# Optimization experiments

Hardware: AMD Instinct MI355X
Metric: run time of the kernel (lower is better)

## Reference

```python
import jax, jax.numpy as jnp
import numpy as np

ATTN_HEADS = 4
NEG = -1e9
LN_EPS = 1e-5


def _ln(x, s, b):
    m = x.mean(-1, keepdims=True)
    v = ((x - m) ** 2).mean(-1, keepdims=True)
    return (x - m) * jax.lax.rsqrt(v + LN_EPS) * s + b


def setup_inputs() -> dict:
    key = jax.random.key(0)
    ks = jax.random.split(key, 40)
    B, L, D, FF, NL = 512, 192, 256, 1024, 2
    V, U, I = 30000, 100000, 50000
    Lp, Ln, NF = 30, 300, 13
    Lu = jax.random.randint(ks[0], (B,), 1, L // 2)
    Li = jax.random.randint(ks[1], (B,), 1, L // 2)
    inp = {
        'attr': jax.random.randint(ks[2], (B, L), 0, V),
        'attr_inds': jax.random.randint(ks[3], (B, L), 0, 3),
        'attr_tf': jax.random.uniform(ks[4], (B, L), dtype=jnp.float32),
        'attr_feat': jax.random.normal(ks[5], (B, L, NF), dtype=jnp.float32),
        'attr_lens': Lu + Li,
        'attr_lens_user': Lu,
        'attr_lens_item': Li,
        'user_ids': jax.random.randint(ks[6], (B,), 0, U),
        'item_ids': jax.random.randint(ks[7], (B,), 0, I),
        'pos_targets': jax.random.randint(ks[8], (B, Lp), 0, V),
        'pos_lens': jax.random.randint(ks[9], (B,), 1, Lp + 1),
        'neg_targets': jax.random.randint(ks[10], (B, Ln), 0, V),
        'neg_lens': jax.random.randint(ks[11], (B,), 1, Ln + 1),
        # embedding tables (uniform(-0.1,0.1) per f_init_weight)
        'attr_emb': jax.random.uniform(ks[12], (V, D), minval=-0.1, maxval=0.1),
        'ind_emb': jax.random.uniform(ks[13], (3, D), minval=-0.1, maxval=0.1),
        'user_emb_table': jax.random.uniform(ks[14], (U, D), minval=-0.1, maxval=0.1),
        'item_emb_table': jax.random.uniform(ks[15], (I, D), minval=-0.1, maxval=0.1),
        'out_emb_user': jax.random.uniform(ks[16], (V, 2 * D), minval=-0.1, maxval=0.1),
        'out_emb_item': jax.random.uniform(ks[17], (V, 2 * D), minval=-0.1, maxval=0.1),
        # attr-weight head: Linear(13,1) + sigmoid
        'feat_w': jax.random.normal(ks[18], (NF,)) * 0.02,
        'feat_b': jnp.zeros(()),
        # transformer encoder params, stacked over NL layers
        'Wqkv': jax.random.normal(ks[19], (NL, 3 * D, D)) * 0.02,
        'bqkv': jnp.zeros((NL, 3 * D)),
        'Wo': jax.random.normal(ks[20], (NL, D, D)) * 0.02,
        'bo': jnp.zeros((NL, D)),
        'ln1_s': jnp.ones((NL, D)), 'ln1_b': jnp.zeros((NL, D)),
        'W1': jax.random.normal(ks[21], (NL, FF, D)) * 0.02,
        'b1': jnp.zeros((NL, FF)),
        'W2': jax.random.normal(ks[22], (NL, D, FF)) * 0.02,
        'b2': jnp.zeros((NL, D)),
        'ln2_s': jnp.ones((NL, D)), 'ln2_b': jnp.zeros((NL, D)),
    }
    return inp


def reference(attr, attr_inds, attr_tf, attr_feat, attr_lens, attr_lens_user,
              attr_lens_item, user_ids, item_ids, pos_targets, pos_lens,
              neg_targets, neg_lens, attr_emb, ind_emb, user_emb_table,
              item_emb_table, out_emb_user, out_emb_item, feat_w, feat_b,
              Wqkv, bqkv, Wo, bo, ln1_s, ln1_b, W1, b1, W2, b2, ln2_s, ln2_b):
    B, L = attr.shape
    D = attr_emb.shape[1]
    NL = Wqkv.shape[0]
    Dh = D // ATTN_HEADS
    pos = jnp.arange(L)
    valid = pos[None, :] < attr_lens[:, None]  # [B,L] True = valid key

    x = attr_emb[attr] + ind_emb[attr_inds]  # [B,L,D]
    for l in range(NL):  # post-LN TransformerEncoderLayer, relu, no dropout
        qkv = x @ Wqkv[l].T + bqkv[l]
        q, k, v = jnp.split(qkv, 3, axis=-1)
        q = q.reshape(B, L, ATTN_HEADS, Dh).transpose(0, 2, 1, 3)
        k = k.reshape(B, L, ATTN_HEADS, Dh).transpose(0, 2, 1, 3)
        v = v.reshape(B, L, ATTN_HEADS, Dh).transpose(0, 2, 1, 3)
        scores = jnp.einsum('bhqd,bhkd->bhqk', q, k) / np.sqrt(Dh).astype(x.dtype)
        scores = jnp.where(valid[:, None, None, :], scores, NEG)
        a = jax.nn.softmax(scores, axis=-1)
        ctx = jnp.einsum('bhqk,bhkd->bhqd', a, v).transpose(0, 2, 1, 3).reshape(B, L, D)
        x = _ln(x + ctx @ Wo[l].T + bo[l], ln1_s[l], ln1_b[l])
        ff = jax.nn.relu(x @ W1[l].T + b1[l]) @ W2[l].T + b2[l]
        x = _ln(x + ff, ln2_s[l], ln2_b[l])

    # ragged weighted segment average over user span [0,Lu) and item span [Lu,Lu+Li)
    w_user = jax.nn.sigmoid(attr_feat @ feat_w + feat_b)  # [B,L]
    wted = x * attr_tf[..., None]
    umask = pos[None, :] < attr_lens_user[:, None]
    imask = (~umask) & (pos[None, :] < (attr_lens_user + attr_lens_item)[:, None])
    user_x = (wted * w_user[..., None] * umask[..., None]).sum(1) / attr_lens_user[:, None].astype(x.dtype)
    item_x = (wted * (1.0 - w_user)[..., None] * imask[..., None]).sum(1) / attr_lens_item[:, None].astype(x.dtype)

    user_out = jnp.concatenate([user_x, user_emb_table[user_ids]], axis=-1)  # [B,2D]
    item_out = jnp.concatenate([item_x, item_emb_table[item_ids]], axis=-1)

    def logit(t):
        return (jnp.einsum('bkd,bd->bk', out_emb_user[t], user_out)
                + jnp.einsum('bkd,bd->bk', out_emb_item[t], item_out))

    pos_logits = logit(pos_targets)
    neg_logits = logit(neg_targets)
    pmask = jnp.arange(pos_targets.shape[1])[None, :] < pos_lens[:, None]
    nmask = jnp.arange(neg_targets.shape[1])[None, :] < neg_lens[:, None]
    logits = jnp.concatenate([pos_logits, neg_logits], axis=-1)
    mask = jnp.concatenate([pmask, nmask], axis=-1)
    new_targets = jnp.concatenate([jnp.ones_like(pos_targets), jnp.zeros_like(neg_targets)], axis=1) * mask
    return logits, mask, new_targets
```

## Files before the change

kernel.cpp:

```cpp
#include <hip/hip_runtime.h>
#include <hip/hip_bf16.h>
#include <cstdint>
#include <cstddef>

#define B_ 512
#define L_ 192
#define D_ 256
#define H_ 4
#define DH_ 64
#define FF_ 1024
#define NL_ 2
#define LP_ 30
#define LNEG_ 300
#define NF_ 13
#define M_ (B_*L_)
#define NT_ 330
#define V_ 30000

typedef __attribute__((ext_vector_type(8))) short bf16x8;
typedef __attribute__((ext_vector_type(4))) float f32x4;

__device__ __forceinline__ ushort f2b(float f) {
  union { float f; uint32_t u; } v; v.f = f;
  uint32_t u = v.u;
  return (ushort)((u + 0x7FFFu + ((u >> 16) & 1u)) >> 16);
}
__device__ __forceinline__ float b2f(ushort u) {
  union { uint32_t u; float f; } v; v.u = (uint32_t)u << 16; return v.f;
}
__device__ __forceinline__ void stage16(const ushort* src, char* dst) {
  __builtin_amdgcn_global_load_lds((const __attribute__((address_space(1))) unsigned int*)src,
                                   (__attribute__((address_space(3))) unsigned int*)dst, 16, 0, 0);
}

__global__ __launch_bounds__(512) void k_prefix(
    const int* __restrict__ lens, int* __restrict__ off,
    int* __restrict__ ccnt, int* __restrict__ ccntp, int Bc, int nchunks)
{
  const int t = threadIdx.x;
  int s = 0;
  for (int i = 0; i < t; ++i) s += lens[i];
  off[t] = s;
  if (t == 511) off[512] = s + lens[511];
  if (t < nchunks) {
    int s2 = 0;
    const int c0 = t * Bc;
    for (int i = 0; i < Bc; ++i) s2 += lens[c0 + i];
    ccnt[t]  = s2;
    ccntp[t] = (s2 + 127) & ~127;
  }
}

__global__ __launch_bounds__(256) void k_f2b(const float* __restrict__ in, ushort* __restrict__ out) {
  const int i = (blockIdx.x*256 + threadIdx.x)*8;
  float4 a = *(const float4*)(in+i);
  float4 b = *(const float4*)(in+i+4);
  ushort4 o1; o1.x=f2b(a.x); o1.y=f2b(a.y); o1.z=f2b(a.z); o1.w=f2b(a.w);
  ushort4 o2; o2.x=f2b(b.x); o2.y=f2b(b.y); o2.z=f2b(b.z); o2.w=f2b(b.w);
  *(ushort4*)(out+i)   = o1;
  *(ushort4*)(out+i+4) = o2;
}

__global__ __launch_bounds__(256) void k_f2b4(
    const float* __restrict__ wq, const float* __restrict__ wo,
    const float* __restrict__ w1, const float* __restrict__ w2,
    ushort* __restrict__ oq, ushort* __restrict__ oo,
    ushort* __restrict__ o1, ushort* __restrict__ o2)
{
  int bb = blockIdx.x;
  const float* in; ushort* out; int base;
  if (bb < 192)      { in = wq; out = oq; base = bb; }
  else if (bb < 256) { in = wo; out = oo; base = bb - 192; }
  else if (bb < 512) { in = w1; out = o1; base = bb - 256; }
  else               { in = w2; out = o2; base = bb - 512; }
  const int i = base*2048 + threadIdx.x*8;
  float4 a = *(const float4*)(in+i);
  float4 b = *(const float4*)(in+i+4);
  ushort4 q1; q1.x=f2b(a.x); q1.y=f2b(a.y); q1.z=f2b(a.z); q1.w=f2b(a.w);
  ushort4 q2; q2.x=f2b(b.x); q2.y=f2b(b.y); q2.z=f2b(b.z); q2.w=f2b(b.w);
  *(ushort4*)(out+i)   = q1;
  *(ushort4*)(out+i+4) = q2;
}

__global__ __launch_bounds__(256) void k_embed(
    const int* __restrict__ attr, const int* __restrict__ inds,
    const int* __restrict__ lens, const int* __restrict__ off,
    const float* __restrict__ attr_emb, const float* __restrict__ ind_emb,
    ushort* __restrict__ xb)
{
  int idx = blockIdx.x*256 + threadIdx.x;
  int token = idx >> 6;
  int c = (idx & 63) * 4;
  int b = token / L_;
  int l = token - b*L_;
  if (l >= lens[b]) return;
  size_t crow = (size_t)off[b] + l;
  int a = attr[token];
  int id = inds[token];
  const float4 e  = *(const float4*)(attr_emb + (size_t)a*D_ + c);
  const float4 ie = *(const float4*)(ind_emb  + (size_t)id*D_ + c);
  ushort4 ob; ob.x=f2b(e.x+ie.x); ob.y=f2b(e.y+ie.y); ob.z=f2b(e.z+ie.z); ob.w=f2b(e.w+ie.w);
  *(ushort4*)(xb + crow*D_ + c) = ob;
}

template<int OUT_BF16, int RELU>
__global__ __launch_bounds__(256) void k_gemm_mfma(
    const ushort* __restrict__ A, const int* __restrict__ aoffp,
    const int* __restrict__ cntp,
    const ushort* __restrict__ W, const float* __restrict__ bias,
    void* __restrict__ Cv, int N, int K)
{
  if ((int)blockIdx.y * 128 >= *cntp) return;
  __shared__ alignas(16) ushort As[8192];
  __shared__ alignas(16) ushort Bs[8192];
  const int abase = *aoffp;
  const int tid = threadIdx.x;
  const int w = tid >> 6, l = tid & 63;
  const int g = l >> 4, c16 = l & 15;
  const int m0 = blockIdx.y*128, n0 = blockIdx.x*128;
  const int wr = w >> 1, wc = w & 1;
  const int swzr = (c16 & 7) << 4;

  f32x4 acc[4][4];
  #pragma unroll
  for (int i=0;i<4;++i)
    #pragma unroll
    for (int j=0;j<4;++j) acc[i][j] = (f32x4){0.f,0.f,0.f,0.f};

  for (int k0=0; k0<K; k0+=64) {
    #pragma unroll
    for (int i=0;i<4;++i) {
      const int li  = i*4096 + tid*16;
      const int row = li >> 7;
      const int col = ((li & 127) ^ ((row & 7) << 4)) >> 1;
      stage16(A + (size_t)(abase+m0+row)*K + k0 + col, (char*)(As) + i*4096 + w*1024);
      stage16(W + (size_t)(n0+row)*K + k0 + col,       (char*)(Bs) + i*4096 + w*1024);
    }
    __syncthreads();
    #pragma unroll
    for (int ks=0; ks<2; ++ks) {
      const int cb = ((g*16 + ks*64) ^ swzr) >> 1;
      bf16x8 af[4], bfr[4];
      #pragma unroll
      for (int i2=0;i2<4;++i2) {
        af[i2]  = *(const bf16x8*)(As + (size_t)(wr*64 + i2*16 + c16)*64 + cb);
        bfr[i2] = *(const bf16x8*)(Bs + (size_t)(wc*64 + i2*16 + c16)*64 + cb);
      }
      #pragma unroll
      for (int mi=0;mi<4;++mi)
        #pragma unroll
        for (int ni=0;ni<4;++ni)
          acc[mi][ni] = __builtin_amdgcn_mfma_f32_16x16x32_bf16(bfr[ni], af[mi], acc[mi][ni], 0,0,0);
    }
    __syncthreads();
  }
  #pragma unroll
  for (int ni=0;ni<4;++ni) {
    const int nc = n0 + wc*64 + ni*16 + 4*g;
    const float4 bv = *(const float4*)(bias + nc);
    #pragma unroll
    for (int mi=0;mi<4;++mi) {
      float v0 = acc[mi][ni][0] + bv.x;
      float v1 = acc[mi][ni][1] + bv.y;
      float v2 = acc[mi][ni][2] + bv.z;
      float v3 = acc[mi][ni][3] + bv.w;
      if (RELU) { v0=fmaxf(v0,0.f); v1=fmaxf(v1,0.f); v2=fmaxf(v2,0.f); v3=fmaxf(v3,0.f); }
      const size_t idx = (size_t)(m0 + wr*64 + mi*16 + c16)*N + nc;
      if (OUT_BF16) {
        ushort4 o; o.x=f2b(v0); o.y=f2b(v1); o.z=f2b(v2); o.w=f2b(v3);
        *(ushort4*)((ushort*)Cv + idx) = o;
      } else {
        float4 o; o.x=v0; o.y=v1; o.z=v2; o.w=v3;
        *(float4*)((float*)Cv + idx) = o;
      }
    }
  }
}

__global__ __launch_bounds__(512) void k_gemm_ln(
    const ushort* __restrict__ A,
    const int* __restrict__ cntp, const int* __restrict__ cnt,
    const int* __restrict__ xoffp,
    const ushort* __restrict__ W,
    const float* __restrict__ bias,
    const float* __restrict__ lns, const float* __restrict__ lnb,
    ushort* __restrict__ xb, int K)
{
  const int m0 = blockIdx.x*128;
  if (m0 >= *cntp) return;
  __shared__ alignas(16) ushort As[8192];
  __shared__ alignas(16) ushort Bs[16384];
  __shared__ float red[4][2][128];
  const int tid = threadIdx.x;
  const int w = tid >> 6, l = tid & 63;
  const int g = l >> 4, c16 = l & 15;
  const int wr = w >> 2, wc = w & 3;
  const int swzr = (c16 & 7) << 4;

  f32x4 acc[4][4];
  #pragma unroll
  for (int i=0;i<4;++i)
    #pragma unroll
    for (int j=0;j<4;++j) acc[i][j] = (f32x4){0.f,0.f,0.f,0.f};

  for (int k0=0; k0<K; k0+=64) {
    #pragma unroll
    for (int i=0;i<2;++i) {
      const int li  = i*8192 + tid*16;
      const int row = li >> 7;
      const int col = ((li & 127) ^ ((row & 7) << 4)) >> 1;
      stage16(A + (size_t)(m0+row)*K + k0 + col, (char*)(As) + i*8192 + w*1024);
    }
    #pragma unroll
    for (int i=0;i<4;++i) {
      const int li  = i*8192 + tid*16;
      const int row = li >> 7;
      const int col = ((li & 127) ^ ((row & 7) << 4)) >> 1;
      stage16(W + (size_t)row*K + k0 + col, (char*)(Bs) + i*8192 + w*1024);
    }
    __syncthreads();
    #pragma unroll
    for (int ks=0; ks<2; ++ks) {
      const int cb = ((g*16 + ks*64) ^ swzr) >> 1;
      bf16x8 af[4], bfr[4];
      #pragma unroll
      for (int i2=0;i2<4;++i2) {
        af[i2]  = *(const bf16x8*)(As + (size_t)(wr*64 + i2*16 + c16)*64 + cb);
        bfr[i2] = *(const bf16x8*)(Bs + (size_t)(wc*64 + i2*16 + c16)*64 + cb);
      }
      #pragma unroll
      for (int mi=0;mi<4;++mi)
        #pragma unroll
        for (int ni=0;ni<4;++ni)
          acc[mi][ni] = __builtin_amdgcn_mfma_f32_16x16x32_bf16(bfr[ni], af[mi], acc[mi][ni], 0,0,0);
    }
    __syncthreads();
  }

  const int xbase = *xoffp + m0;
  float4 bv[4], sv[4], bb[4];
  #pragma unroll
  for (int ni=0;ni<4;++ni) {
    const int nc = wc*64 + ni*16 + 4*g;
    bv[ni] = *(const float4*)(bias + nc);
    sv[ni] = *(const float4*)(lns + nc);
    bb[ni] = *(const float4*)(lnb + nc);
  }
  float ps[4], pq[4];
  #pragma unroll
  for (int mi=0;mi<4;++mi) {
    ps[mi]=0.f; pq[mi]=0.f;
    const int lrow = wr*64 + mi*16 + c16;
    const ushort* xr = xb + (size_t)(xbase + lrow)*256;
    #pragma unroll
    for (int ni=0;ni<4;++ni) {
      const int nc = wc*64 + ni*16 + 4*g;
      ushort4 rx = *(const ushort4*)(xr + nc);
      float y0 = acc[mi][ni][0] + bv[ni].x + b2f(rx.x);
      float y1 = acc[mi][ni][1] + bv[ni].y + b2f(rx.y);
      float y2 = acc[mi][ni][2] + bv[ni].z + b2f(rx.z);
      float y3 = acc[mi][ni][3] + bv[ni].w + b2f(rx.w);
      acc[mi][ni][0]=y0; acc[mi][ni][1]=y1; acc[mi][ni][2]=y2; acc[mi][ni][3]=y3;
      ps[mi] += (y0+y1)+(y2+y3);
      pq[mi] += (y0*y0+y1*y1)+(y2*y2+y3*y3);
    }
  }
  #pragma unroll
  for (int mi=0;mi<4;++mi) {
    ps[mi] += __shfl_xor(ps[mi], 16, 64);
    pq[mi] += __shfl_xor(pq[mi], 16, 64);
    ps[mi] += __shfl_xor(ps[mi], 32, 64);
    pq[mi] += __shfl_xor(pq[mi], 32, 64);
  }
  if (g == 0) {
    #pragma unroll
    for (int mi=0;mi<4;++mi) {
      const int lrow = wr*64 + mi*16 + c16;
      red[wc][0][lrow] = ps[mi];
      red[wc][1][lrow] = pq[mi];
    }
  }
  __syncthreads();
  const int cexact = *cnt;
  #pragma unroll
  for (int mi=0;mi<4;++mi) {
    const int lrow = wr*64 + mi*16 + c16;
    float tsum = red[0][0][lrow] + red[1][0][lrow] + red[2][0][lrow] + red[3][0][lrow];
    float tsq  = red[0][1][lrow] + red[1][1][lrow] + red[2][1][lrow] + red[3][1][lrow];
    float mean = tsum * (1.f/256.f);
    float var  = tsq * (1.f/256.f) - mean*mean;
    float inv  = rsqrtf(var + 1e-5f);
    if (m0 + lrow < cexact) {
      ushort* xbr = xb + (size_t)(xbase + lrow)*256;
      #pragma unroll
      for (int ni=0;ni<4;++ni) {
        const int nc = wc*64 + ni*16 + 4*g;
        ushort4 o;
        o.x = f2b((acc[mi][ni][0]-mean)*inv*sv[ni].x + bb[ni].x);
        o.y = f2b((acc[mi][ni][1]-mean)*inv*sv[ni].y + bb[ni].y);
        o.z = f2b((acc[mi][ni][2]-mean)*inv*sv[ni].z + bb[ni].z);
        o.w = f2b((acc[mi][ni][3]-mean)*inv*sv[ni].w + bb[ni].w);
        *(ushort4*)(xbr + nc) = o;
      }
    }
  }
}

__global__ __launch_bounds__(512) void k_ffn(
    const int* __restrict__ cntp, const int* __restrict__ cnt,
    const int* __restrict__ xoffp,
    const ushort* __restrict__ W1, const float* __restrict__ b1,
    const ushort* __restrict__ W2, const float* __restrict__ b2,
    const float* __restrict__ lns, const float* __restrict__ lnb,
    ushort* __restrict__ xb)
{
  const int m0 = blockIdx.x*64;
  if (m0 >= *cntp) return;
  __shared__ alignas(16) char lds[81920];
  char* Xs = lds;
  char* Wb = lds + 32768;
  char* Hs = lds + 65536;
  float* red = (float*)(lds + 32768);
  const int tid = threadIdx.x;
  const int w = tid >> 6, l = tid & 63;
  const int g = l >> 4, c16 = l & 15;
  const int wr = w >> 2, wc = w & 3;
  const int swzr = (c16 & 7) << 4;
  const int xbase = *xoffp + m0;

  int tokl[2];
  #pragma unroll
  for (int mi=0;mi<2;++mi) tokl[mi] = wr*32 + mi*16 + c16;

  #pragma unroll
  for (int i=0;i<4;++i) {
    const int li = i*8192 + tid*16;
    const int row = li >> 9;
    const int colb = (li & 511) ^ ((row & 7) << 4);
    stage16(xb + (size_t)(xbase+row)*256 + (colb>>1), Xs + i*8192 + w*1024);
  }
  #pragma unroll
  for (int i=0;i<2;++i) {
    const int li = i*8192 + tid*16;
    const int row = li >> 7;
    const int colb = (li & 127) ^ ((row & 7) << 4);
    stage16(W1 + (size_t)row*256 + (colb>>1), Wb + i*8192 + w*1024);
  }
  __syncthreads();

  f32x4 tac[2][4];
  #pragma unroll
  for (int i=0;i<2;++i)
    #pragma unroll
    for (int j=0;j<4;++j) tac[i][j] = (f32x4){0.f,0.f,0.f,0.f};

  int pp = 0;
  for (int s=0; s<8; ++s) {
    f32x4 hac[2][2];
    #pragma unroll
    for (int i=0;i<2;++i)
      #pragma unroll
      for (int j=0;j<2;++j) hac[i][j] = (f32x4){0.f,0.f,0.f,0.f};

    #pragma unroll
    for (int kc=0; kc<4; ++kc) {
      char* cur = Wb + pp*16384;
      char* nxt = Wb + (pp^1)*16384;
      if (kc < 3) {
        #pragma unroll
        for (int i=0;i<2;++i) {
          const int li = i*8192 + tid*16;
          const int row = li >> 7;
          const int colb = (li & 127) ^ ((row & 7) << 4);
          stage16(W1 + (size_t)(s*128+row)*256 + (kc+1)*64 + (colb>>1), nxt + i*8192 + w*1024);
        }
      } else {
        #pragma unroll
        for (int i=0;i<2;++i) {
          const int li = i*8192 + tid*16;
          const int row = li >> 7;
          const int colb = (li & 127) ^ ((row & 7) << 4);
          stage16(W2 + (size_t)row*1024 + s*128 + (colb>>1), nxt + i*8192 + w*1024);
        }
      }
      #pragma unroll
      for (int ks=0; ks<2; ++ks) {
        const int cbw = (ks*64 + g*16) ^ swzr;
        bf16x8 w1f[2], xf[2];
        #pragma unroll
        for (int ni=0;ni<2;++ni)
          w1f[ni] = *(const bf16x8*)(cur + (wc*32 + ni*16 + c16)*128 + cbw);
        #pragma unroll
        for (int mi=0;mi<2;++mi)
          xf[mi] = *(const bf16x8*)(Xs + tokl[mi]*512 + ((kc*128 + ks*64 + g*16) ^ swzr));
        #pragma unroll
        for (int mi=0;mi<2;++mi)
          #pragma unroll
          for (int ni=0;ni<2;++ni)
            hac[mi][ni] = __builtin_amdgcn_mfma_f32_16x16x32_bf16(w1f[ni], xf[mi], hac[mi][ni], 0,0,0);
      }
      if (kc == 3) {
        #pragma unroll
        for (int ni=0;ni<2;++ni) {
          const int ffc = wc*32 + ni*16 + 4*g;
          const float4 bb1 = *(const float4*)(b1 + s*128 + ffc);
          #pragma unroll
          for (int mi=0;mi<2;++mi) {
            ushort4 o;
            o.x = f2b(fmaxf(hac[mi][ni][0] + bb1.x, 0.f));
            o.y = f2b(fmaxf(hac[mi][ni][1] + bb1.y, 0.f));
            o.z = f2b(fmaxf(hac[mi][ni][2] + bb1.z, 0.f));
            o.w = f2b(fmaxf(hac[mi][ni][3] + bb1.w, 0.f));
            *(ushort4*)(Hs + tokl[mi]*256 + ((ffc*2) ^ swzr)) = o;
          }
        }
      }
      __syncthreads();
      pp ^= 1;
    }

    #pragma unroll
    for (int t2=0; t2<4; ++t2) {
      const int dh = t2 >> 1, kc2 = t2 & 1;
      char* cur = Wb + pp*16384;
      char* nxt = Wb + (pp^1)*16384;
      if (t2 < 3) {
        const int nd = (t2+1) >> 1, nk = (t2+1) & 1;
        #pragma unroll
        for (int i=0;i<2;++i) {
          const int li = i*8192 + tid*16;
          const int row = li >> 7;
          const int colb = (li & 127) ^ ((row & 7) << 4);
          stage16(W2 + (size_t)(nd*128+row)*1024 + s*128 + nk*64 + (colb>>1), nxt + i*8192 + w*1024);
        }
      } else if (s < 7) {
        #pragma unroll
        for (int i=0;i<2;++i) {
          const int li = i*8192 + tid*16;
          const int row = li >> 7;
          const int colb = (li & 127) ^ ((row & 7) << 4);
          stage16(W1 + (size_t)((s+1)*128+row)*256 + (colb>>1), nxt + i*8192 + w*1024);
        }
      }
      #pragma unroll
      for (int ks=0; ks<2; ++ks) {
        const int cbw = (ks*64 + g*16) ^ swzr;
        bf16x8 w2f[2], hf[2];
        #pragma unroll
        for (int ni=0;ni<2;++ni)
          w2f[ni] = *(const bf16x8*)(cur + (wc*32 + ni*16 + c16)*128 + cbw);
        #pragma unroll
        for (int mi=0;mi<2;++mi)
          hf[mi] = *(const bf16x8*)(Hs + tokl[mi]*256 + ((kc2*128 + ks*64 + g*16) ^ swzr));
        #pragma unroll
        for (int mi=0;mi<2;++mi)
          #pragma unroll
          for (int ni=0;ni<2;++ni)
            tac[mi][dh*2+ni] = __builtin_amdgcn_mfma_f32_16x16x32_bf16(w2f[ni], hf[mi], tac[mi][dh*2+ni], 0,0,0);
      }
      __syncthreads();
      pp ^= 1;
    }
  }

  float4 bv[4], sv[4], bb[4];
  #pragma unroll
  for (int n=0;n<4;++n) {
    const int nc = (n>>1)*128 + wc*32 + (n&1)*16 + 4*g;
    bv[n] = *(const float4*)(b2 + nc);
    sv[n] = *(const float4*)(lns + nc);
    bb[n] = *(const float4*)(lnb + nc);
  }
  float ps[2], pq[2];
  #pragma unroll
  for (int mi=0;mi<2;++mi) {
    ps[mi]=0.f; pq[mi]=0.f;
    const ushort* xr = xb + (size_t)(xbase + tokl[mi])*256;
    #pragma unroll
    for (int n=0;n<4;++n) {
      const int nc = (n>>1)*128 + wc*32 + (n&1)*16 + 4*g;
      ushort4 rx = *(const ushort4*)(xr + nc);
      float y0 = tac[mi][n][0] + bv[n].x + b2f(rx.x);
      float y1 = tac[mi][n][1] + bv[n].y + b2f(rx.y);
      float y2 = tac[mi][n][2] + bv[n].z + b2f(rx.z);
      float y3 = tac[mi][n][3] + bv[n].w + b2f(rx.w);
      tac[mi][n][0]=y0; tac[mi][n][1]=y1; tac[mi][n][2]=y2; tac[mi][n][3]=y3;
      ps[mi] += (y0+y1)+(y2+y3);
      pq[mi] += (y0*y0+y1*y1)+(y2*y2+y3*y3);
    }
  }
  #pragma unroll
  for (int mi=0;mi<2;++mi) {
    ps[mi] += __shfl_xor(ps[mi], 16, 64);
    pq[mi] += __shfl_xor(pq[mi], 16, 64);
    ps[mi] += __shfl_xor(ps[mi], 32, 64);
    pq[mi] += __shfl_xor(pq[mi], 32, 64);
  }
  if (g == 0) {
    #pragma unroll
    for (int mi=0;mi<2;++mi) {
      red[(wc*2+0)*64 + tokl[mi]] = ps[mi];
      red[(wc*2+1)*64 + tokl[mi]] = pq[mi];
    }
  }
  __syncthreads();
  const int cexact = *cnt;
  #pragma unroll
  for (int mi=0;mi<2;++mi) {
    const int lrow = tokl[mi];
    float tsum = red[0*64+lrow] + red[2*64+lrow] + red[4*64+lrow] + red[6*64+lrow];
    float tsq  = red[1*64+lrow] + red[3*64+lrow] + red[5*64+lrow] + red[7*64+lrow];
    float mean = tsum * (1.f/256.f);
    float var  = tsq * (1.f/256.f) - mean*mean;
    float inv  = rsqrtf(var + 1e-5f);
    if (m0 + lrow < cexact) {
      ushort* xbr = xb + (size_t)(xbase + lrow)*256;
      #pragma unroll
      for (int n=0;n<4;++n) {
        const int nc = (n>>1)*128 + wc*32 + (n&1)*16 + 4*g;
        ushort4 o;
        o.x = f2b((tac[mi][n][0]-mean)*inv*sv[n].x + bb[n].x);
        o.y = f2b((tac[mi][n][1]-mean)*inv*sv[n].y + bb[n].y);
        o.z = f2b((tac[mi][n][2]-mean)*inv*sv[n].z + bb[n].z);
        o.w = f2b((tac[mi][n][3]-mean)*inv*sv[n].w + bb[n].w);
        *(ushort4*)(xbr + nc) = o;
      }
    }
  }
}

__global__ __launch_bounds__(256) void k_attn_mfma(
    const ushort* __restrict__ qkv, ushort* __restrict__ ctx,
    const int* __restrict__ offc)
{
  __shared__ alignas(16) char lds[81920];
  char* Kb = lds;
  char* Vt = lds + 24576;
  const int tid = threadIdx.x;
  const int w = tid >> 6, l = tid & 63;
  const int g = l >> 4, c = l & 15;
  char* Pw = lds + 57344 + w*6144;
  const int bl = blockIdx.x >> 2, h = blockIdx.x & 3;
  const int rowbase = offc[bl] - offc[0];
  const int len = offc[bl+1] - offc[bl];
  const int nkt = (len + 15) >> 4;
  const int nkf = (len + 31) >> 5;
  const ushort* base = qkv + (size_t)rowbase*768;
  ushort* cbase = ctx + (size_t)rowbase*256;

  const int lenk8 = nkt*16*8;
  for (int idx = tid; idx < lenk8; idx += 256) {
    int row = idx >> 3, ch = idx & 7;
    uint4 v = *(const uint4*)(base + (size_t)row*768 + 256 + h*64 + ch*8);
    *(uint4*)(Kb + ((row*128 + ch*16) ^ ((row&7)<<4))) = v;
  }
  {
    const int lenv = nkf*32;
    int d0 = (tid & 15)*4;
    for (int key = tid >> 4; key < lenv; key += 16) {
      ushort4 v = *(const ushort4*)(base + (size_t)key*768 + 512 + h*64 + d0);
      ushort vv[4] = {v.x, v.y, v.z, v.w};
      #pragma unroll
      for (int j=0;j<4;++j) {
        int d = d0 + j;
        *(ushort*)(Vt + ((d*512 + key*2) ^ ((d&7)<<4))) = vv[j];
      }
    }
  }
  __syncthreads();

  for (int t = nkt; t < 2*nkf; ++t) {
    #pragma unroll
    for (int r=0;r<4;++r) {
      int q = 4*g + r;
      *(ushort*)(Pw + (((t>>1)*1024 + q*64 + ((t&1)*16 + c)*2) ^ (((q>>2)&3)<<4))) = 0;
    }
  }

  const int nst = (len + 15) >> 4;
  for (int s = w; s < nst; s += 4) {
    const ushort* qp = base + (size_t)(s*16 + c)*768 + h*64 + g*8;
    bf16x8 aq0 = *(const bf16x8*)qp;
    bf16x8 aq1 = *(const bf16x8*)(qp + 32);

    f32x4 sc[12];
    #pragma unroll
    for (int t=0;t<12;++t) {
      sc[t] = (f32x4){0.f,0.f,0.f,0.f};
      if (t < nkt) {
        int ba0 = ((t*16 + c)*128 + g*16)      ^ ((c&7)<<4);
        int ba1 = ((t*16 + c)*128 + g*16 + 64) ^ ((c&7)<<4);
        bf16x8 k0 = *(const bf16x8*)(Kb + ba0);
        bf16x8 k1 = *(const bf16x8*)(Kb + ba1);
        sc[t] = __builtin_amdgcn_mfma_f32_16x16x32_bf16(aq0, k0, sc[t], 0,0,0);
        sc[t] = __builtin_amdgcn_mfma_f32_16x16x32_bf16(aq1, k1, sc[t], 0,0,0);
        if (t == nkt-1 && t*16 + c >= len)
          sc[t] = (f32x4){-1e30f,-1e30f,-1e30f,-1e30f};
      }
    }
    float mr[4] = {-1e30f,-1e30f,-1e30f,-1e30f};
    #pragma unroll
    for (int t=0;t<12;++t) if (t<nkt) {
      #pragma unroll
      for (int r=0;r<4;++r) mr[r] = fmaxf(mr[r], sc[t][r]);
    }
    #pragma unroll
    for (int r=0;r<4;++r) {
      mr[r] = fmaxf(mr[r], __shfl_xor(mr[r], 1, 16));
      mr[r] = fmaxf(mr[r], __shfl_xor(mr[r], 2, 16));
      mr[r] = fmaxf(mr[r], __shfl_xor(mr[r], 4, 16));
      mr[r] = fmaxf(mr[r], __shfl_xor(mr[r], 8, 16));
    }
    float sr[4] = {0.f,0.f,0.f,0.f};
    #pragma unroll
    for (int t=0;t<12;++t) if (t<nkt) {
      #pragma unroll
      for (int r=0;r<4;++r) {
        float p = __expf((sc[t][r] - mr[r]) * 0.125f);
        sr[r] += p;
        int q = 4*g + r;
        *(ushort*)(Pw + (((t>>1)*1024 + q*64 + ((t&1)*16 + c)*2) ^ (((q>>2)&3)<<4))) = f2b(p);
      }
    }
    #pragma unroll
    for (int r=0;r<4;++r) {
      sr[r] += __shfl_xor(sr[r], 1, 16);
      sr[r] += __shfl_xor(sr[r], 2, 16);
      sr[r] += __shfl_xor(sr[r], 4, 16);
      sr[r] += __shfl_xor(sr[r], 8, 16);
    }
    f32x4 oa[4];
    #pragma unroll
    for (int dt=0;dt<4;++dt) oa[dt] = (f32x4){0.f,0.f,0.f,0.f};
    #pragma unroll
    for (int kf=0;kf<6;++kf) if (kf<nkf) {
      bf16x8 pf = *(const bf16x8*)(Pw + ((kf*1024 + c*64 + g*16) ^ (((c>>2)&3)<<4)));
      #pragma unroll
      for (int dt=0;dt<4;++dt) {
        int d = dt*16 + c;
        bf16x8 vf = *(const bf16x8*)(Vt + ((d*512 + kf*64 + g*16) ^ ((d&7)<<4)));
        oa[dt] = __builtin_amdgcn_mfma_f32_16x16x32_bf16(pf, vf, oa[dt], 0,0,0);
      }
    }
    float inv[4];
    #pragma unroll
    for (int r=0;r<4;++r) inv[r] = 1.f / sr[r];
    ushort* orow = cbase + (size_t)(s*16)*256 + h*64;
    #pragma unroll
    for (int r=0;r<4;++r) {
      int q = 4*g + r;
      if (s*16 + q < len) {
        #pragma unroll
        for (int dt=0;dt<4;++dt)
          orow[(size_t)q*256 + dt*16 + c] = f2b(oa[dt][r] * inv[r]);
      }
    }
  }
}

__global__ __launch_bounds__(256) void k_pool(
    const ushort* __restrict__ xb, const int* __restrict__ off,
    const float* __restrict__ attr_tf, const float* __restrict__ attr_feat,
    const int* __restrict__ lens_u, const int* __restrict__ lens_i,
    const int* __restrict__ user_ids, const int* __restrict__ item_ids,
    const float* __restrict__ user_tab, const float* __restrict__ item_tab,
    const float* __restrict__ feat_w, const float* __restrict__ feat_b,
    float* __restrict__ user_out, float* __restrict__ item_out)
{
  __shared__ float wu[L_], tf[L_];
  const int b = blockIdx.x;
  const int t = threadIdx.x;
  if (t < L_) {
    const float* f = attr_feat + ((size_t)b*L_ + t)*NF_;
    float sacc = feat_b[0];
    #pragma unroll
    for (int j=0;j<NF_;++j) sacc = fmaf(f[j], feat_w[j], sacc);
    wu[t] = 1.f/(1.f+__expf(-sacc));
    tf[t] = attr_tf[b*L_+t];
  }
  __syncthreads();
  const int Lu = lens_u[b], Li = lens_i[b];
  const ushort* xrow = xb + (size_t)off[b]*D_;
  float su=0.f, si=0.f;
  for (int l=0;l<Lu+Li;++l) {
    float val = b2f(xrow[(size_t)l*D_ + t]) * tf[l];
    if (l < Lu) su = fmaf(val, wu[l], su);
    else        si = fmaf(val, 1.f-wu[l], si);
  }
  user_out[(size_t)b*512 + t]       = su/(float)Lu;
  item_out[(size_t)b*512 + t]       = si/(float)Li;
  user_out[(size_t)b*512 + 256 + t] = user_tab[(size_t)user_ids[b]*D_ + t];
  item_out[(size_t)b*512 + 256 + t] = item_tab[(size_t)item_ids[b]*D_ + t];
}

__global__ __launch_bounds__(256) void k_logits(
    const int* __restrict__ pos_t, const int* __restrict__ neg_t,
    const int* __restrict__ pos_l, const int* __restrict__ neg_l,
    const ushort* __restrict__ oeu, const ushort* __restrict__ oei,
    const float* __restrict__ user_out, const float* __restrict__ item_out,
    float* __restrict__ out)
{
  const int g = blockIdx.x*4 + (threadIdx.x >> 6);
  const int lane = threadIdx.x & 63;
  const int b = g / NT_;
  const int k = g - b*NT_;
  const int tid_ = (k < LP_) ? pos_t[b*LP_ + k] : neg_t[b*LNEG_ + (k-LP_)];
  const ushort* eu = oeu + (size_t)tid_*512;
  const ushort* ei = oei + (size_t)tid_*512;
  const float* uo = user_out + (size_t)b*512;
  const float* io = item_out + (size_t)b*512;
  const int d0 = lane*8;
  float s = 0.f;
  ushort4 a0 = *(const ushort4*)(eu+d0), a1 = *(const ushort4*)(eu+d0+4);
  float4 u0 = *(const float4*)(uo+d0), u1 = *(const float4*)(uo+d0+4);
  s += b2f(a0.x)*u0.x + b2f(a0.y)*u0.y + b2f(a0.z)*u0.z + b2f(a0.w)*u0.w;
  s += b2f(a1.x)*u1.x + b2f(a1.y)*u1.y + b2f(a1.z)*u1.z + b2f(a1.w)*u1.w;
  ushort4 c0 = *(const ushort4*)(ei+d0), c1 = *(const ushort4*)(ei+d0+4);
  float4 i0 = *(const float4*)(io+d0), i1 = *(const float4*)(io+d0+4);
  s += b2f(c0.x)*i0.x + b2f(c0.y)*i0.y + b2f(c0.z)*i0.z + b2f(c0.w)*i0.w;
  s += b2f(c1.x)*i1.x + b2f(c1.y)*i1.y + b2f(c1.z)*i1.z + b2f(c1.w)*i1.w;
  #pragma unroll
  for (int off=32; off>0; off>>=1) s += __shfl_xor(s, off, 64);
  if (lane == 0) {
    out[(size_t)b*NT_ + k] = s;
    float mv, nt;
    if (k < LP_) { mv = (k < pos_l[b]) ? 1.f : 0.f; nt = mv; }
    else         { mv = ((k - LP_) < neg_l[b]) ? 1.f : 0.f; nt = 0.f; }
    out[(size_t)B_*NT_   + (size_t)b*NT_ + k] = mv;
    out[(size_t)2*B_*NT_ + (size_t)b*NT_ + k] = nt;
  }
}

extern "C" void kernel_launch(void* const* d_in, const int* in_sizes, int n_in,
                              void* d_out, int out_size, void* d_ws, size_t ws_size,
                              hipStream_t stream)
{
  const int*   attr      = (const int*)d_in[0];
  const int*   attr_inds = (const int*)d_in[1];
  const float* attr_tf   = (const float*)d_in[2];
  const float* attr_feat = (const float*)d_in[3];
  const int*   attr_lens = (const int*)d_in[4];
  const int*   lens_u    = (const int*)d_in[5];
  const int*   lens_i    = (const int*)d_in[6];
  const int*   user_ids  = (const int*)d_in[7];
  const int*   item_ids  = (const int*)d_in[8];
  const int*   pos_t     = (const int*)d_in[9];
  const int*   pos_l     = (const int*)d_in[10];
  const int*   neg_t     = (const int*)d_in[11];
  const int*   neg_l     = (const int*)d_in[12];
  const float* attr_emb  = (const float*)d_in[13];
  const float* ind_emb   = (const float*)d_in[14];
  const float* user_tab  = (const float*)d_in[15];
  const float* item_tab  = (const float*)d_in[16];
  const float* oeu       = (const float*)d_in[17];
  const float* oei       = (const float*)d_in[18];
  const float* feat_w    = (const float*)d_in[19];
  const float* feat_b    = (const float*)d_in[20];
  const float* Wqkv      = (const float*)d_in[21];
  const float* bqkv      = (const float*)d_in[22];
  const float* Wo        = (const float*)d_in[23];
  const float* bo        = (const float*)d_in[24];
  const float* ln1s      = (const float*)d_in[25];
  const float* ln1b      = (const float*)d_in[26];
  const float* W1        = (const float*)d_in[27];
  const float* b1        = (const float*)d_in[28];
  const float* W2        = (const float*)d_in[29];
  const float* b2        = (const float*)d_in[30];
  const float* ln2s      = (const float*)d_in[31];
  const float* ln2b      = (const float*)d_in[32];

  int* ioff  = (int*)d_ws;
  int* ccnt  = ioff + 520;
  int* ccntp = ccnt + 64;
  float* ws = (float*)d_ws + 768;
  float* uo = ws;
  float* io = uo + (size_t)B_*512;
  ushort* xb   = (ushort*)(io + (size_t)B_*512);
  ushort* wq_b = xb + (size_t)M_*D_;
  ushort* wo_b = wq_b + (size_t)2*768*256;
  ushort* w1_b = wo_b + (size_t)2*256*256;
  ushort* w2_b = w1_b + (size_t)2*1024*256;
  ushort* oeu_b = w2_b + (size_t)2*256*1024;
  ushort* oei_b = oeu_b + (size_t)V_*512;
  float* scratch = (float*)(oei_b + (size_t)V_*512);

  const size_t fixed_floats = 768 + (size_t)B_*1024 + (size_t)M_*(D_/2) + 786432 + (size_t)V_*512;
  int Bc = 8;
  for (int cand = 512; cand >= 8; cand >>= 1) {
    size_t need = (fixed_floats + (size_t)cand*L_*512) * sizeof(float);
    if (need <= ws_size) { Bc = cand; break; }
  }
  const int nchunks = B_ / Bc;
  const size_t Mc = (size_t)Bc * L_;

  float* out = (float*)d_out;

  k_prefix<<<1, 512, 0, stream>>>(attr_lens, ioff, ccnt, ccntp, Bc, nchunks);
  k_f2b4<<<768, 256, 0, stream>>>(Wqkv, Wo, W1, W2, wq_b, wo_b, w1_b, w2_b);
  k_f2b<<<(V_*512)/2048, 256, 0, stream>>>(oeu, oeu_b);
  k_f2b<<<(V_*512)/2048, 256, 0, stream>>>(oei, oei_b);
  k_embed<<<M_*64/256, 256, 0, stream>>>(attr, attr_inds, attr_lens, ioff, attr_emb, ind_emb, xb);

  for (int l=0; l<NL_; ++l) {
    const float* bqkv_l = bqkv + (size_t)l*768;
    const float* bo_l   = bo   + (size_t)l*D_;
    const float* b1_l   = b1   + (size_t)l*FF_;
    const float* b2_l   = b2   + (size_t)l*D_;
    for (int c=0; c<nchunks; ++c) {
      const int* offc = ioff + c*Bc;
      const int* cntp = ccntp + c;
      const int* cnt  = ccnt + c;
      ushort* qkv_b = (ushort*)scratch;
      ushort* ctx_b = (ushort*)(scratch + Mc*384);

      k_gemm_mfma<1,0><<<dim3(768/128, Mc/128), 256, 0, stream>>>(
          xb, offc, cntp, wq_b + (size_t)l*768*256, bqkv_l, qkv_b, 768, 256);
      k_attn_mfma<<<Bc*H_, 256, 0, stream>>>(qkv_b, ctx_b, offc);
      k_gemm_ln<<<Mc/128, 512, 0, stream>>>(
          ctx_b, cntp, cnt, offc, wo_b + (size_t)l*256*256, bo_l,
          ln1s + (size_t)l*D_, ln1b + (size_t)l*D_, xb, 256);
      k_ffn<<<Mc/64, 512, 0, stream>>>(
          cntp, cnt, offc, w1_b + (size_t)l*1024*256, b1_l,
          w2_b + (size_t)l*256*1024, b2_l,
          ln2s + (size_t)l*D_, ln2b + (size_t)l*D_, xb);
    }
  }
  k_pool<<<B_, 256, 0, stream>>>(xb, ioff, attr_tf, attr_feat, lens_u, lens_i, user_ids, item_ids,
                                 user_tab, item_tab, feat_w, feat_b, uo, io);
  k_logits<<<B_*NT_/4, 256, 0, stream>>>(pos_t, neg_t, pos_l, neg_l, oeu_b, oei_b, uo, io, out);
}
```

Measured before the change: 634.8 us.

## Triple-buffer FFN weight staging with two-chunk lookahead and partial vmcnt waits

The FFN kernel's weight staging goes from double to triple buffering in LDS. Chunks are prefetched two steps ahead, and each step waits with s_waitcnt vmcnt(2) instead of a full __syncthreads drain, so global loads overlap more with MFMA work. The W1 and W2 phases are merged into one 8-step loop per FF slice. LDS use grows from 80KB to 96KB, which may reduce occupancy. Correctness now depends on the manual vmcnt counting matching the number of outstanding loads.

Measured after the change: 640.3 us. About the same (+0.9%).

```diff
diff --git a/kernel.cpp b/kernel.cpp
--- a/kernel.cpp
+++ b/kernel.cpp
@@ -316,10 +316,10 @@
 {
   const int m0 = blockIdx.x*64;
   if (m0 >= *cntp) return;
-  __shared__ alignas(16) char lds[81920];
+  __shared__ alignas(16) char lds[98304];
   char* Xs = lds;
   char* Wb = lds + 32768;
-  char* Hs = lds + 65536;
+  char* Hs = lds + 81920;
   float* red = (float*)(lds + 32768);
   const int tid = threadIdx.x;
   const int w = tid >> 6, l = tid & 63;
@@ -332,6 +332,22 @@
   #pragma unroll
   for (int mi=0;mi<2;++mi) tokl[mi] = wr*32 + mi*16 + c16;
 
+  auto stage_chunk = [&](int s, int q, char* dst) {
+    #pragma unroll
+    for (int i=0;i<2;++i) {
+      const int li = i*8192 + tid*16;
+      const int row = li >> 7;
+      const int colb = (li & 127) ^ ((row & 7) << 4);
+      const ushort* src;
+      if (q < 4) src = W1 + (size_t)(s*128+row)*256 + q*64 + (colb>>1);
+      else {
+        const int t2 = q - 4;
+        src = W2 + (size_t)((t2>>1)*128+row)*1024 + s*128 + (t2&1)*64 + (colb>>1);
+      }
+      stage16(src, dst + i*8192 + w*1024);
+    }
+  };
+
   #pragma unroll
   for (int i=0;i<4;++i) {
     const int li = i*8192 + tid*16;
@@ -339,14 +355,11 @@
     const int colb = (li & 511) ^ ((row & 7) << 4);
     stage16(xb + (size_t)(xbase+row)*256 + (colb>>1), Xs + i*8192 + w*1024);
   }
-  #pragma unroll
-  for (int i=0;i<2;++i) {
-    const int li = i*8192 + tid*16;
-    const int row = li >> 7;
-    const int colb = (li & 127) ^ ((row & 7) << 4);
-    stage16(W1 + (size_t)row*256 + (colb>>1), Wb + i*8192 + w*1024);
-  }
-  __syncthreads();
+  stage_chunk(0, 0, Wb);
+  stage_chunk(0, 1, Wb + 16384);
+  asm volatile("s_waitcnt vmcnt(2) lgkmcnt(0)" ::: "memory");
+  __builtin_amdgcn_s_barrier();
+  __builtin_amdgcn_sched_barrier(0);
 
   f32x4 tac[2][4];
   #pragma unroll
@@ -354,7 +367,7 @@
     #pragma unroll
     for (int j=0;j<4;++j) tac[i][j] = (f32x4){0.f,0.f,0.f,0.f};
 
-  int pp = 0;
+  int cur = 0;
   for (int s=0; s<8; ++s) {
     f32x4 hac[2][2];
     #pragma unroll
@@ -363,103 +376,76 @@
       for (int j=0;j<2;++j) hac[i][j] = (f32x4){0.f,0.f,0.f,0.f};
 
     #pragma unroll
-    for (int kc=0; kc<4; ++kc) {
-      char* cur = Wb + pp*16384;
-      char* nxt = Wb + (pp^1)*16384;
-      if (kc < 3) {
+    for (int q=0; q<8; ++q) {
+      if (q < 6) {
+        stage_chunk(s, q+2, Wb + ((cur+2)%3)*16384);
+      } else if (s < 7) {
+        stage_chunk(s+1, q-6, Wb + ((cur+2)%3)*16384);
+      }
+      char* curbuf = Wb + cur*16384;
+
+      if (q < 4) {
         #pragma unroll
-        for (int i=0;i<2;++i) {
-          const int li = i*8192 + tid*16;
-          const int row = li >> 7;
-          const int colb = (li & 127) ^ ((row & 7) << 4);
-          stage16(W1 + (size_t)(s*128+row)*256 + (kc+1)*64 + (colb>>1), nxt + i*8192 + w*1024);
+        for (int ks=0; ks<2; ++ks) {
+          const int cbw = (ks*64 + g*16) ^ swzr;
+          bf16x8 w1f[2], xf[2];
+          #pragma unroll
+          for (int ni=0;ni<2;++ni)
+            w1f[ni] = *(const bf16x8*)(curbuf + (wc*32 + ni*16 + c16)*128 + cbw);
+          #pragma unroll
+          for (int mi=0;mi<2;++mi)
+            xf[mi] = *(const bf16x8*)(Xs + tokl[mi]*512 + ((q*128 + ks*64 + g*16) ^ swzr));
+          #pragma unroll
+          for (int mi=0;mi<2;++mi)
+            #pragma unroll
+            for (int ni=0;ni<2;++ni)
+              hac[mi][ni] = __builtin_amdgcn_mfma_f32_16x16x32_bf16(w1f[ni], xf[mi], hac[mi][ni], 0,0,0);
+        }
+        if (q == 3) {
+          #pragma unroll
+          for (int ni=0;ni<2;++ni) {
+            const int ffc = wc*32 + ni*16 + 4*g;
+            const float4 bb1 = *(const float4*)(b1 + s*128 + ffc);
+            #pragma unroll
+            for (int mi=0;mi<2;++mi) {
+              ushort4 o;
+              o.x = f2b(fmaxf(hac[mi][ni][0] + bb1.x, 0.f));
+              o.y = f2b(fmaxf(hac[mi][ni][1] + bb1.y, 0.f));
+              o.z = f2b(fmaxf(hac[mi][ni][2] + bb1.z, 0.f));
+              o.w = f2b(fmaxf(hac[mi][ni][3] + bb1.w, 0.f));
+              *(ushort4*)(Hs + tokl[mi]*256 + ((ffc*2) ^ swzr)) = o;
+            }
+          }
         }
       } else {
+        const int dh = (q-4) >> 1, kc2 = (q-4) & 1;
         #pragma unroll
-        for (int i=0;i<2;++i) {
-          const int li = i*8192 + tid*16;
-          const int row = li >> 7;
-          const int colb = (li & 127) ^ ((row & 7) << 4);
-          stage16(W2 + (size_t)row*1024 + s*128 + (colb>>1), nxt + i*8192 + w*1024);
-        }
-      }
-      #pragma unroll
-      for (int ks=0; ks<2; ++ks) {
-        const int cbw = (ks*64 + g*16) ^ swzr;
-        bf16x8 w1f[2], xf[2];
-        #pragma unroll
-        for (int ni=0;ni<2;++ni)
-          w1f[ni] = *(const bf16x8*)(cur + (wc*32 + ni*16 + c16)*128 + cbw);
-        #pragma unroll
-        for (int mi=0;mi<2;++mi)
-          xf[mi] = *(const bf16x8*)(Xs + tokl[mi]*512 + ((kc*128 + ks*64 + g*16) ^ swzr));
-        #pragma unroll
-        for (int mi=0;mi<2;++mi)
+        for (int ks=0; ks<2; ++ks) {
+          const int cbw = (ks*64 + g*16) ^ swzr;
+          bf16x8 w2f[2], hf[2];
           #pragma unroll
           for (int ni=0;ni<2;++ni)
-            hac[mi][ni] = __builtin_amdgcn_mfma_f32_16x16x32_bf16(w1f[ni], xf[mi], hac[mi][ni], 0,0,0);
-      }
-      if (kc == 3) {
-        #pragma unroll
-        for (int ni=0;ni<2;++ni) {
-          const int ffc = wc*32 + ni*16 + 4*g;
-          const float4 bb1 = *(const float4*)(b1 + s*128 + ffc);
+            w2f[ni] = *(const bf16x8*)(curbuf + (wc*32 + ni*16 + c16)*128 + cbw);
           #pragma unroll
-          for (int mi=0;mi<2;++mi) {
-            ushort4 o;
-            o.x = f2b(fmaxf(hac[mi][ni][0] + bb1.x, 0.f));
-            o.y = f2b(fmaxf(hac[mi][ni][1] + bb1.y, 0.f));
-            o.z = f2b(fmaxf(hac[mi][ni][2] + bb1.z, 0.f));
-            o.w = f2b(fmaxf(hac[mi][ni][3] + bb1.w, 0.f));
-            *(ushort4*)(Hs + tokl[mi]*256 + ((ffc*2) ^ swzr)) = o;
-          }
+          for (int mi=0;mi<2;++mi)
+            hf[mi] = *(const bf16x8*)(Hs + tokl[mi]*256 + ((kc2*128 + ks*64 + g*16) ^ swzr));
+          #pragma unroll
+          for (int mi=0;mi<2;++mi)
+            #pragma unroll
+            for (int ni=0;ni<2;++ni)
+              tac[mi][dh*2+ni] = __builtin_amdgcn_mfma_f32_16x16x32_bf16(w2f[ni], hf[mi], tac[mi][dh*2+ni], 0,0,0);
         }
       }
-      __syncthreads();
-      pp ^= 1;
-    }
-
-    #pragma unroll
-    for (int t2=0; t2<4; ++t2) {
-      const int dh = t2 >> 1, kc2 = t2 & 1;
-      char* cur = Wb + pp*16384;
-      char* nxt = Wb + (pp^1)*16384;
-      if (t2 < 3) {
-        const int nd = (t2+1) >> 1, nk = (t2+1) & 1;
-        #pragma unroll
-        for (int i=0;i<2;++i) {
-          const int li = i*8192 + tid*16;
-          const int row = li >> 7;
-          const int colb = (li & 127) ^ ((row & 7) << 4);
-          stage16(W2 + (size_t)(nd*128+row)*1024 + s*128 + nk*64 + (colb>>1), nxt + i*8192 + w*1024);
-        }
-      } else if (s < 7) {
-        #pragma unroll
-        for (int i=0;i<2;++i) {
-          const int li = i*8192 + tid*16;
-          const int row = li >> 7;
-          const int colb = (li & 127) ^ ((row & 7) << 4);
-          stage16(W1 + (size_t)((s+1)*128+row)*256 + (colb>>1), nxt + i*8192 + w*1024);
-        }
-      }
-      #pragma unroll
-      for (int ks=0; ks<2; ++ks) {
-        const int cbw = (ks*64 + g*16) ^ swzr;
-        bf16x8 w2f[2], hf[2];
-        #pragma unroll
-        for (int ni=0;ni<2;++ni)
-          w2f[ni] = *(const bf16x8*)(cur + (wc*32 + ni*16 + c16)*128 + cbw);
-        #pragma unroll
-        for (int mi=0;mi<2;++mi)
-          hf[mi] = *(const bf16x8*)(Hs + tokl[mi]*256 + ((kc2*128 + ks*64 + g*16) ^ swzr));
-        #pragma unroll
-        for (int mi=0;mi<2;++mi)
-          #pragma unroll
-          for (int ni=0;ni<2;++ni)
-            tac[mi][dh*2+ni] = __builtin_amdgcn_mfma_f32_16x16x32_bf16(w2f[ni], hf[mi], tac[mi][dh*2+ni], 0,0,0);
-      }
-      __syncthreads();
-      pp ^= 1;
+
+      if (q >= 6) {
+        if (s == 7) { asm volatile("s_waitcnt vmcnt(0) lgkmcnt(0)" ::: "memory"); }
+        else        { asm volatile("s_waitcnt vmcnt(2) lgkmcnt(0)" ::: "memory"); }
+      } else {
+        asm volatile("s_waitcnt vmcnt(2) lgkmcnt(0)" ::: "memory");
+      }
+      __builtin_amdgcn_s_barrier();
+      __builtin_amdgcn_sched_barrier(0);
+      cur = (cur + 1) % 3;
     }
   }
 
```
